# Optimization experiments

Measured on AMD Instinct MI355X. Metric: run time of the kernel, lower is better.

## Reference

```python
import jax, jax.numpy as jnp
import numpy as np

EMBED_DIM = 768
NUM_HEADS = 32
B = 4
N = 512


def setup_inputs() -> dict:
    key = jax.random.key(0)
    ks = jax.random.split(key, 11)
    s = 0.02  # param init scale
    E = EMBED_DIM
    return {
        "query": jax.random.normal(ks[0], (B, N, E), jnp.float32),
        "attn_bias": jax.random.normal(ks[1], (B * NUM_HEADS, N, N), jnp.float32),
        "delta_pos": jax.random.normal(ks[2], (B, N, N, 3), jnp.float32),
        "Wq": jax.random.normal(ks[3], (E, E), jnp.float32) * s,
        "bq": jnp.zeros((E,), jnp.float32),
        "Wk": jax.random.normal(ks[4], (E, E), jnp.float32) * s,
        "bk": jnp.zeros((E,), jnp.float32),
        "Wv": jax.random.normal(ks[5], (E, E), jnp.float32) * s,
        "bv": jnp.zeros((E,), jnp.float32),
        # force_proj{1,2,3} stacked: row c is the Linear(E,1) weight for axis c
        "Wf": jax.random.normal(ks[6], (3, E), jnp.float32) * s,
        "bf": jnp.zeros((3,), jnp.float32),
    }


def reference(query, attn_bias, delta_pos, Wq, bq, Wk, bk, Wv, bv, Wf, bf):
    b, n, e = query.shape
    h = NUM_HEADS
    d = e // h
    scaling = d ** (-0.5)
    # projections -> (b, h, n, d)
    q = (query @ Wq.T + bq).reshape(b, n, h, d).transpose(0, 2, 1, 3) * scaling
    k = (query @ Wk.T + bk).reshape(b, n, h, d).transpose(0, 2, 1, 3)
    v = (query @ Wv.T + bv).reshape(b, n, h, d).transpose(0, 2, 1, 3)
    # attention scores + bias; dropout is identity in eval mode (p=0.1, training=False)
    attn = jnp.einsum("bhnd,bhmd->bhnm", q, k) + attn_bias.reshape(b, h, n, n)
    probs = jax.nn.softmax(attn, axis=-1)  # (b,h,n,m)
    # rotate probs by delta_pos (c in {x,y,z}) and contract with v over m
    # x[b,n,c,h,d] = sum_m probs[b,h,n,m] * delta_pos[b,n,m,c] * v[b,h,m,d]
    x = jnp.einsum("bhnm,bnmc,bhmd->bnchd", probs, delta_pos, v).reshape(b, n, 3, e)
    # per-axis force projection: Linear(E,1) for each spatial axis
    force = jnp.einsum("bnce,ce->bnc", x, Wf) + bf
    return force.astype(jnp.float32)
```

## Files before the change

kernel.cpp:

```cpp
#include <hip/hip_runtime.h>
#include <hip/hip_bf16.h>
#include <cstdint>
#include <cstddef>

#define EMBED 768
#define NHEAD 32
#define HDIM 24
#define DPAD 32
#define BATCH 4
#define SEQ 512
#define WCOLS 1632
#define NPADCOL 1664

typedef __attribute__((ext_vector_type(8))) short short8;
typedef __attribute__((ext_vector_type(4))) short short4v;
typedef __attribute__((ext_vector_type(4))) float f32x4;

static __device__ __forceinline__ unsigned short f2b(float v) {
    __hip_bfloat16 h = __float2bfloat16(v);
    return *reinterpret_cast<unsigned short*>(&h);
}

__global__ __launch_bounds__(256) void prep_w_kernel(
    const float* __restrict__ Wq, const float* __restrict__ Wk,
    const float* __restrict__ Wv, const float* __restrict__ Wf,
    unsigned short* __restrict__ WcT)
{
    const float sc = 0.20412414523193154f;
    int j = blockIdx.x;
    #pragma unroll
    for (int rep = 0; rep < 3; ++rep) {
        int e = rep * 256 + threadIdx.x;
        float v;
        if (j < 768) {
            v = Wq[(size_t)j * EMBED + e] * sc;
        } else if (j < 1536) {
            v = Wk[(size_t)(j - 768) * EMBED + e];
        } else if (j < WCOLS) {
            int jc = j - 1536, h = jc / 3, c = jc - h * 3;
            float s = 0.f;
            #pragma unroll
            for (int d = 0; d < HDIM; ++d)
                s = fmaf(Wv[(size_t)(h * HDIM + d) * EMBED + e],
                         Wf[c * EMBED + h * HDIM + d], s);
            v = s;
        } else {
            v = 0.f;
        }
        WcT[(size_t)j * EMBED + e] = f2b(v);
    }
}

__global__ __launch_bounds__(256) void prep_b_kernel(
    const float* __restrict__ bq, const float* __restrict__ bk,
    const float* __restrict__ bv, const float* __restrict__ Wf,
    float* __restrict__ bcat)
{
    int j = blockIdx.x * 256 + threadIdx.x;
    if (j >= NPADCOL) return;
    float v = 0.f;
    if (j < 768) v = bq[j] * 0.20412414523193154f;
    else if (j < 1536) v = bk[j - 768];
    else if (j < WCOLS) {
        int jc = j - 1536, h = jc / 3, c = jc - h * 3;
        float s = 0.f;
        #pragma unroll
        for (int d = 0; d < HDIM; ++d)
            s = fmaf(bv[h * HDIM + d], Wf[c * EMBED + h * HDIM + d], s);
        v = s;
    }
    bcat[j] = v;
}

__global__ __launch_bounds__(256) void qconv_kernel(
    const float* __restrict__ q, unsigned short* __restrict__ o)
{
    size_t i = ((size_t)blockIdx.x * 256 + threadIdx.x) * 8;
    float4 a = *(const float4*)(q + i);
    float4 b = *(const float4*)(q + i + 4);
    union { unsigned short u[8]; short8 v; } r;
    r.u[0] = f2b(a.x); r.u[1] = f2b(a.y); r.u[2] = f2b(a.z); r.u[3] = f2b(a.w);
    r.u[4] = f2b(b.x); r.u[5] = f2b(b.y); r.u[6] = f2b(b.z); r.u[7] = f2b(b.w);
    *(short8*)(o + i) = r.v;
}

#define LSTR 36
__global__ __launch_bounds__(256) void gemm_kernel(
    const unsigned short* __restrict__ Aq, const unsigned short* __restrict__ WcT,
    const float* __restrict__ bcat,
    unsigned short* __restrict__ qp, unsigned short* __restrict__ kp,
    float* __restrict__ vwb)
{
    __shared__ short As[64 * LSTR];
    __shared__ short Bs[64 * LSTR];
    int t = threadIdx.x;
    int lane = t & 63, wv = t >> 6;
    int l15 = lane & 15, lg = lane >> 4;
    int m0 = blockIdx.x * 64, n0 = blockIdx.y * 64;
    int wm = (wv >> 1) * 32, wn = (wv & 1) * 32;

    f32x4 acc[2][2];
    #pragma unroll
    for (int i = 0; i < 2; ++i)
        #pragma unroll
        for (int j = 0; j < 2; ++j) acc[i][j] = (f32x4){0.f, 0.f, 0.f, 0.f};

    const unsigned short* Ag = Aq + (size_t)(m0 + (t >> 2)) * EMBED + (t & 3) * 8;
    const unsigned short* Bg = WcT + (size_t)(n0 + (t >> 2)) * EMBED + (t & 3) * 8;
    int lidx = (t >> 2) * LSTR + (t & 3) * 8;

    for (int kt = 0; kt < EMBED / 32; ++kt) {
        short8 av = *(const short8*)(Ag + kt * 32);
        short8 bv = *(const short8*)(Bg + kt * 32);
        __syncthreads();
        union { short4v h[2]; short8 v; } ua, ub;
        ua.v = av; ub.v = bv;
        *(short4v*)&As[lidx] = ua.h[0]; *(short4v*)&As[lidx + 4] = ua.h[1];
        *(short4v*)&Bs[lidx] = ub.h[0]; *(short4v*)&Bs[lidx + 4] = ub.h[1];
        __syncthreads();
        short8 af[2], bfr[2];
        #pragma unroll
        for (int i = 0; i < 2; ++i) {
            int ra = (wm + i * 16 + l15) * LSTR + lg * 8;
            int rb = (wn + i * 16 + l15) * LSTR + lg * 8;
            union { short4v h[2]; short8 v; } u1, u2;
            u1.h[0] = *(const short4v*)&As[ra]; u1.h[1] = *(const short4v*)&As[ra + 4];
            u2.h[0] = *(const short4v*)&Bs[rb]; u2.h[1] = *(const short4v*)&Bs[rb + 4];
            af[i] = u1.v; bfr[i] = u2.v;
        }
        #pragma unroll
        for (int mt = 0; mt < 2; ++mt)
            #pragma unroll
            for (int nt = 0; nt < 2; ++nt)
                acc[mt][nt] = __builtin_amdgcn_mfma_f32_16x16x32_bf16(
                    af[mt], bfr[nt], acc[mt][nt], 0, 0, 0);
    }

    #pragma unroll
    for (int mt = 0; mt < 2; ++mt) {
        #pragma unroll
        for (int nt = 0; nt < 2; ++nt) {
            #pragma unroll
            for (int r = 0; r < 4; ++r) {
                int gm = m0 + wm + mt * 16 + lg * 4 + r;
                int gn = n0 + wn + nt * 16 + l15;
                float v = acc[mt][nt][r] + bcat[gn];
                int b = gm >> 9, ns = gm & 511;
                if (gn < 768) {
                    int h = gn / 24, d = gn - h * 24;
                    qp[((size_t)(b * NHEAD + h) * SEQ + ns) * DPAD + d] = f2b(v);
                } else if (gn < 1536) {
                    int j2 = gn - 768, h = j2 / 24, d = j2 - h * 24;
                    kp[((size_t)(b * NHEAD + h) * SEQ + ns) * DPAD + d] = f2b(v);
                } else if (gn < WCOLS) {
                    int jc = gn - 1536, h = jc / 3, c = jc - h * 3;
                    vwb[((size_t)(b * NHEAD + h) * 3 + c) * SEQ + ns] = v;
                }
            }
        }
    }
}

__global__ __launch_bounds__(256) void init_out_kernel(
    const float* __restrict__ bf, float* __restrict__ out)
{
    int i = blockIdx.x * 256 + threadIdx.x;
    if (i < BATCH * SEQ * 3) out[i] = bf[i - (i / 3) * 3];
}

__global__ __launch_bounds__(512, 4) void attn_kernel(
    const unsigned short* __restrict__ qp, const unsigned short* __restrict__ kp,
    const float* __restrict__ vwb, const float* __restrict__ bias,
    const float* __restrict__ delta, float* __restrict__ out)
{
    __shared__ float denp[2][8][16];
    __shared__ float facp[8][16][3];
    int t = threadIdx.x, lane = t & 63, w = t >> 6;
    int l15 = lane & 15, lg = lane >> 4;
    int nbase = blockIdx.x * 16;
    int b = blockIdx.y;
    int hg = blockIdx.z;
    int mbase = w * 64;

    float dreg[4][4][3];
    #pragma unroll
    for (int r = 0; r < 4; ++r)
        #pragma unroll
        for (int tl = 0; tl < 4; ++tl) {
            const float* dp = delta +
                ((size_t)(b * SEQ + nbase + lg * 4 + r) * SEQ + mbase + tl * 16 + l15) * 3;
            dreg[r][tl][0] = dp[0]; dreg[r][tl][1] = dp[1]; dreg[r][tl][2] = dp[2];
        }

    float fac[4][3];
    #pragma unroll
    for (int r = 0; r < 4; ++r) { fac[r][0] = 0.f; fac[r][1] = 0.f; fac[r][2] = 0.f; }

    for (int hh = 0; hh < 8; ++hh) {
        int bh = b * NHEAD + hg * 8 + hh;
        short8 aq = *(const short8*)(qp + ((size_t)bh * SEQ + nbase + l15) * DPAD + lg * 8);
        f32x4 acc[4];
        #pragma unroll
        for (int tl = 0; tl < 4; ++tl) {
            short8 bk = *(const short8*)(kp +
                ((size_t)bh * SEQ + mbase + tl * 16 + l15) * DPAD + lg * 8);
            f32x4 z = {0.f, 0.f, 0.f, 0.f};
            acc[tl] = __builtin_amdgcn_mfma_f32_16x16x32_bf16(aq, bk, z, 0, 0, 0);
        }
        float ep[4][4];
        float dpart[4] = {0.f, 0.f, 0.f, 0.f};
        #pragma unroll
        for (int tl = 0; tl < 4; ++tl)
            #pragma unroll
            for (int r = 0; r < 4; ++r) {
                float s = acc[tl][r] + bias[
                    ((size_t)bh * SEQ + nbase + lg * 4 + r) * SEQ + mbase + tl * 16 + l15];
                float e = __expf(s);
                ep[tl][r] = e;
                dpart[r] += e;
            }
        #pragma unroll
        for (int r = 0; r < 4; ++r)
            #pragma unroll
            for (int o = 1; o <= 8; o <<= 1)
                dpart[r] += __shfl_xor(dpart[r], o);
        int buf = hh & 1;
        if (l15 == 0) {
            #pragma unroll
            for (int r = 0; r < 4; ++r) denp[buf][w][lg * 4 + r] = dpart[r];
        }
        __syncthreads();
        float rden[4];
        #pragma unroll
        for (int r = 0; r < 4; ++r) {
            float s = 0.f;
            #pragma unroll
            for (int ww = 0; ww < 8; ++ww) s += denp[buf][ww][lg * 4 + r];
            rden[r] = __builtin_amdgcn_rcpf(s);
        }
        #pragma unroll
        for (int tl = 0; tl < 4; ++tl) {
            #pragma unroll
            for (int c = 0; c < 3; ++c) {
                float vv = vwb[((size_t)bh * 3 + c) * SEQ + mbase + tl * 16 + l15];
                #pragma unroll
                for (int r = 0; r < 4; ++r)
                    fac[r][c] = fmaf(ep[tl][r] * rden[r] * vv, dreg[r][tl][c], fac[r][c]);
            }
        }
    }

    #pragma unroll
    for (int r = 0; r < 4; ++r)
        #pragma unroll
        for (int c = 0; c < 3; ++c) {
            float v = fac[r][c];
            #pragma unroll
            for (int o = 1; o <= 8; o <<= 1) v += __shfl_xor(v, o);
            fac[r][c] = v;
        }
    if (l15 == 0) {
        #pragma unroll
        for (int r = 0; r < 4; ++r)
            #pragma unroll
            for (int c = 0; c < 3; ++c) facp[w][lg * 4 + r][c] = fac[r][c];
    }
    __syncthreads();
    if (t < 48) {
        int n = t / 3, c = t - (t / 3) * 3;
        float s = 0.f;
        #pragma unroll
        for (int ww = 0; ww < 8; ++ww) s += facp[ww][n][c];
        atomicAdd(&out[(size_t)(b * SEQ + nbase + n) * 3 + c], s);
    }
}

extern "C" void kernel_launch(void* const* d_in, const int* in_sizes, int n_in,
                              void* d_out, int out_size, void* d_ws, size_t ws_size,
                              hipStream_t stream)
{
    const float* query = (const float*)d_in[0];
    const float* attn_bias = (const float*)d_in[1];
    const float* delta = (const float*)d_in[2];
    const float* Wq = (const float*)d_in[3];
    const float* bq = (const float*)d_in[4];
    const float* Wk = (const float*)d_in[5];
    const float* bk = (const float*)d_in[6];
    const float* Wv = (const float*)d_in[7];
    const float* bv = (const float*)d_in[8];
    const float* Wf = (const float*)d_in[9];
    const float* bf = (const float*)d_in[10];
    float* out = (float*)d_out;

    uint8_t* p = (uint8_t*)d_ws;
    unsigned short* qp   = (unsigned short*)p; p += (size_t)BATCH * NHEAD * SEQ * DPAD * 2;
    unsigned short* kp   = (unsigned short*)p; p += (size_t)BATCH * NHEAD * SEQ * DPAD * 2;
    unsigned short* qb16 = (unsigned short*)p; p += (size_t)BATCH * SEQ * EMBED * 2;
    unsigned short* WcT  = (unsigned short*)p; p += (size_t)NPADCOL * EMBED * 2;
    float* bcat = (float*)p;                   p += (size_t)NPADCOL * 4;
    float* vwb  = (float*)p;                   p += (size_t)BATCH * NHEAD * 3 * SEQ * 4;

    hipMemsetAsync(qp, 0, (size_t)BATCH * NHEAD * SEQ * DPAD * 2 * 2, stream);

    hipLaunchKernelGGL(prep_w_kernel, dim3(NPADCOL), dim3(256), 0, stream,
                       Wq, Wk, Wv, Wf, WcT);
    hipLaunchKernelGGL(prep_b_kernel, dim3(7), dim3(256), 0, stream,
                       bq, bk, bv, Wf, bcat);
    hipLaunchKernelGGL(qconv_kernel, dim3((BATCH * SEQ * EMBED) / (256 * 8)),
                       dim3(256), 0, stream, query, qb16);
    hipLaunchKernelGGL(gemm_kernel, dim3((BATCH * SEQ) / 64, NPADCOL / 64),
                       dim3(256), 0, stream, qb16, WcT, bcat, qp, kp, vwb);
    hipLaunchKernelGGL(init_out_kernel, dim3((BATCH * SEQ * 3 + 255) / 256),
                       dim3(256), 0, stream, bf, out);
    hipLaunchKernelGGL(attn_kernel, dim3(SEQ / 16, BATCH, 4), dim3(512), 0, stream,
                       qp, kp, vwb, attn_bias, delta, out);
}
```

Baseline: 259.7 us.

## Restructure attention per-head-per-wave, transpose delta_pos, fuse prep and conversion kernels

```diff
diff --git a/kernel.cpp b/kernel.cpp
--- a/kernel.cpp
+++ b/kernel.cpp
@@ -13,7 +13,6 @@
 #define NPADCOL 1664
 
 typedef __attribute__((ext_vector_type(8))) short short8;
-typedef __attribute__((ext_vector_type(4))) short short4v;
 typedef __attribute__((ext_vector_type(4))) float f32x4;
 
 static __device__ __forceinline__ unsigned short f2b(float v) {
@@ -24,7 +23,9 @@
 __global__ __launch_bounds__(256) void prep_w_kernel(
     const float* __restrict__ Wq, const float* __restrict__ Wk,
     const float* __restrict__ Wv, const float* __restrict__ Wf,
-    unsigned short* __restrict__ WcT)
+    const float* __restrict__ bq, const float* __restrict__ bkv,
+    const float* __restrict__ bv,
+    unsigned short* __restrict__ WcT, float* __restrict__ bcat)
 {
     const float sc = 0.20412414523193154f;
     int j = blockIdx.x;
@@ -49,50 +50,46 @@
         }
         WcT[(size_t)j * EMBED + e] = f2b(v);
     }
-}
-
-__global__ __launch_bounds__(256) void prep_b_kernel(
-    const float* __restrict__ bq, const float* __restrict__ bk,
-    const float* __restrict__ bv, const float* __restrict__ Wf,
-    float* __restrict__ bcat)
-{
-    int j = blockIdx.x * 256 + threadIdx.x;
-    if (j >= NPADCOL) return;
-    float v = 0.f;
-    if (j < 768) v = bq[j] * 0.20412414523193154f;
-    else if (j < 1536) v = bk[j - 768];
-    else if (j < WCOLS) {
-        int jc = j - 1536, h = jc / 3, c = jc - h * 3;
-        float s = 0.f;
-        #pragma unroll
-        for (int d = 0; d < HDIM; ++d)
-            s = fmaf(bv[h * HDIM + d], Wf[c * EMBED + h * HDIM + d], s);
-        v = s;
-    }
-    bcat[j] = v;
-}
-
-__global__ __launch_bounds__(256) void qconv_kernel(
-    const float* __restrict__ q, unsigned short* __restrict__ o)
-{
-    size_t i = ((size_t)blockIdx.x * 256 + threadIdx.x) * 8;
-    float4 a = *(const float4*)(q + i);
-    float4 b = *(const float4*)(q + i + 4);
-    union { unsigned short u[8]; short8 v; } r;
-    r.u[0] = f2b(a.x); r.u[1] = f2b(a.y); r.u[2] = f2b(a.z); r.u[3] = f2b(a.w);
-    r.u[4] = f2b(b.x); r.u[5] = f2b(b.y); r.u[6] = f2b(b.z); r.u[7] = f2b(b.w);
-    *(short8*)(o + i) = r.v;
-}
-
-#define LSTR 36
+    if (threadIdx.x == 0) {
+        float v = 0.f;
+        if (j < 768) v = bq[j] * sc;
+        else if (j < 1536) v = bkv[j - 768];
+        else if (j < WCOLS) {
+            int jc = j - 1536, h = jc / 3, c = jc - h * 3;
+            float s = 0.f;
+            #pragma unroll
+            for (int d = 0; d < HDIM; ++d)
+                s = fmaf(bv[h * HDIM + d], Wf[c * EMBED + h * HDIM + d], s);
+            v = s;
+        }
+        bcat[j] = v;
+    }
+}
+
+__global__ __launch_bounds__(256) void dtr_kernel(
+    const float* __restrict__ delta, float* __restrict__ dtr)
+{
+    size_t u = (size_t)blockIdx.x * 256 + threadIdx.x;
+    int m = (int)(u & 511);
+    int n = (int)((u >> 9) & 511);
+    int b = (int)(u >> 18);
+    float d0 = delta[u * 3 + 0];
+    float d1 = delta[u * 3 + 1];
+    float d2 = delta[u * 3 + 2];
+    dtr[((size_t)(b * 3 + 0) * SEQ + n) * SEQ + m] = d0;
+    dtr[((size_t)(b * 3 + 1) * SEQ + n) * SEQ + m] = d1;
+    dtr[((size_t)(b * 3 + 2) * SEQ + n) * SEQ + m] = d2;
+}
+
+#define LSTR 40
 __global__ __launch_bounds__(256) void gemm_kernel(
-    const unsigned short* __restrict__ Aq, const unsigned short* __restrict__ WcT,
+    const float* __restrict__ Aq, const unsigned short* __restrict__ WcT,
     const float* __restrict__ bcat,
     unsigned short* __restrict__ qp, unsigned short* __restrict__ kp,
     float* __restrict__ vwb)
 {
-    __shared__ short As[64 * LSTR];
-    __shared__ short Bs[64 * LSTR];
+    __shared__ short As[2][64 * LSTR];
+    __shared__ short Bs[2][64 * LSTR];
     int t = threadIdx.x;
     int lane = t & 63, wv = t >> 6;
     int l15 = lane & 15, lg = lane >> 4;
@@ -105,28 +102,43 @@
         #pragma unroll
         for (int j = 0; j < 2; ++j) acc[i][j] = (f32x4){0.f, 0.f, 0.f, 0.f};
 
-    const unsigned short* Ag = Aq + (size_t)(m0 + (t >> 2)) * EMBED + (t & 3) * 8;
-    const unsigned short* Bg = WcT + (size_t)(n0 + (t >> 2)) * EMBED + (t & 3) * 8;
-    int lidx = (t >> 2) * LSTR + (t & 3) * 8;
+    int sr = t >> 2;
+    int sc8 = (t & 3) * 8;
+    const float* Ag = Aq + (size_t)(m0 + sr) * EMBED + sc8;
+    const unsigned short* Bg = WcT + (size_t)(n0 + sr) * EMBED + sc8;
+    int lidx = sr * LSTR + sc8;
+
+    short8 fa, fb;
+    {
+        float4 a0 = *(const float4*)(Ag);
+        float4 a1 = *(const float4*)(Ag + 4);
+        union { unsigned short u[8]; short8 v; } r;
+        r.u[0] = f2b(a0.x); r.u[1] = f2b(a0.y); r.u[2] = f2b(a0.z); r.u[3] = f2b(a0.w);
+        r.u[4] = f2b(a1.x); r.u[5] = f2b(a1.y); r.u[6] = f2b(a1.z); r.u[7] = f2b(a1.w);
+        fa = r.v;
+        fb = *(const short8*)(Bg);
+    }
+    *(short8*)&As[0][lidx] = fa;
+    *(short8*)&Bs[0][lidx] = fb;
+    __syncthreads();
 
     for (int kt = 0; kt < EMBED / 32; ++kt) {
-        short8 av = *(const short8*)(Ag + kt * 32);
-        short8 bv = *(const short8*)(Bg + kt * 32);
-        __syncthreads();
-        union { short4v h[2]; short8 v; } ua, ub;
-        ua.v = av; ub.v = bv;
-        *(short4v*)&As[lidx] = ua.h[0]; *(short4v*)&As[lidx + 4] = ua.h[1];
-        *(short4v*)&Bs[lidx] = ub.h[0]; *(short4v*)&Bs[lidx + 4] = ub.h[1];
-        __syncthreads();
+        int cur = kt & 1;
+        bool more = (kt + 1) < EMBED / 32;
+        if (more) {
+            float4 a0 = *(const float4*)(Ag + (kt + 1) * 32);
+            float4 a1 = *(const float4*)(Ag + (kt + 1) * 32 + 4);
+            fb = *(const short8*)(Bg + (size_t)(kt + 1) * 32);
+            union { unsigned short u[8]; short8 v; } r;
+            r.u[0] = f2b(a0.x); r.u[1] = f2b(a0.y); r.u[2] = f2b(a0.z); r.u[3] = f2b(a0.w);
+            r.u[4] = f2b(a1.x); r.u[5] = f2b(a1.y); r.u[6] = f2b(a1.z); r.u[7] = f2b(a1.w);
+            fa = r.v;
+        }
         short8 af[2], bfr[2];
         #pragma unroll
         for (int i = 0; i < 2; ++i) {
-            int ra = (wm + i * 16 + l15) * LSTR + lg * 8;
-            int rb = (wn + i * 16 + l15) * LSTR + lg * 8;
-            union { short4v h[2]; short8 v; } u1, u2;
-            u1.h[0] = *(const short4v*)&As[ra]; u1.h[1] = *(const short4v*)&As[ra + 4];
-            u2.h[0] = *(const short4v*)&Bs[rb]; u2.h[1] = *(const short4v*)&Bs[rb + 4];
-            af[i] = u1.v; bfr[i] = u2.v;
+            af[i]  = *(const short8*)&As[cur][(wm + i * 16 + l15) * LSTR + lg * 8];
+            bfr[i] = *(const short8*)&Bs[cur][(wn + i * 16 + l15) * LSTR + lg * 8];
         }
         #pragma unroll
         for (int mt = 0; mt < 2; ++mt)
@@ -134,6 +146,11 @@
             for (int nt = 0; nt < 2; ++nt)
                 acc[mt][nt] = __builtin_amdgcn_mfma_f32_16x16x32_bf16(
                     af[mt], bfr[nt], acc[mt][nt], 0, 0, 0);
+        if (more) {
+            *(short8*)&As[cur ^ 1][lidx] = fa;
+            *(short8*)&Bs[cur ^ 1][lidx] = fb;
+            __syncthreads();
+        }
     }
 
     #pragma unroll
@@ -168,109 +185,76 @@
     if (i < BATCH * SEQ * 3) out[i] = bf[i - (i / 3) * 3];
 }
 
-__global__ __launch_bounds__(512, 4) void attn_kernel(
+__global__ __launch_bounds__(512) void attn_kernel(
     const unsigned short* __restrict__ qp, const unsigned short* __restrict__ kp,
     const float* __restrict__ vwb, const float* __restrict__ bias,
-    const float* __restrict__ delta, float* __restrict__ out)
-{
-    __shared__ float denp[2][8][16];
-    __shared__ float facp[8][16][3];
+    const float* __restrict__ dtr, float* __restrict__ out)
+{
+    __shared__ float wred[8][16][3];
     int t = threadIdx.x, lane = t & 63, w = t >> 6;
     int l15 = lane & 15, lg = lane >> 4;
     int nbase = blockIdx.x * 16;
     int b = blockIdx.y;
-    int hg = blockIdx.z;
-    int mbase = w * 64;
-
-    float dreg[4][4][3];
-    #pragma unroll
-    for (int r = 0; r < 4; ++r)
-        #pragma unroll
-        for (int tl = 0; tl < 4; ++tl) {
-            const float* dp = delta +
-                ((size_t)(b * SEQ + nbase + lg * 4 + r) * SEQ + mbase + tl * 16 + l15) * 3;
-            dreg[r][tl][0] = dp[0]; dreg[r][tl][1] = dp[1]; dreg[r][tl][2] = dp[2];
-        }
-
-    float fac[4][3];
-    #pragma unroll
-    for (int r = 0; r < 4; ++r) { fac[r][0] = 0.f; fac[r][1] = 0.f; fac[r][2] = 0.f; }
-
-    for (int hh = 0; hh < 8; ++hh) {
-        int bh = b * NHEAD + hg * 8 + hh;
-        short8 aq = *(const short8*)(qp + ((size_t)bh * SEQ + nbase + l15) * DPAD + lg * 8);
-        f32x4 acc[4];
-        #pragma unroll
-        for (int tl = 0; tl < 4; ++tl) {
-            short8 bk = *(const short8*)(kp +
-                ((size_t)bh * SEQ + mbase + tl * 16 + l15) * DPAD + lg * 8);
-            f32x4 z = {0.f, 0.f, 0.f, 0.f};
-            acc[tl] = __builtin_amdgcn_mfma_f32_16x16x32_bf16(aq, bk, z, 0, 0, 0);
-        }
-        float ep[4][4];
-        float dpart[4] = {0.f, 0.f, 0.f, 0.f};
-        #pragma unroll
-        for (int tl = 0; tl < 4; ++tl)
-            #pragma unroll
-            for (int r = 0; r < 4; ++r) {
-                float s = acc[tl][r] + bias[
-                    ((size_t)bh * SEQ + nbase + lg * 4 + r) * SEQ + mbase + tl * 16 + l15];
-                float e = __expf(s);
-                ep[tl][r] = e;
-                dpart[r] += e;
-            }
-        #pragma unroll
-        for (int r = 0; r < 4; ++r)
-            #pragma unroll
-            for (int o = 1; o <= 8; o <<= 1)
-                dpart[r] += __shfl_xor(dpart[r], o);
-        int buf = hh & 1;
-        if (l15 == 0) {
-            #pragma unroll
-            for (int r = 0; r < 4; ++r) denp[buf][w][lg * 4 + r] = dpart[r];
-        }
-        __syncthreads();
-        float rden[4];
+    int bh = b * NHEAD + blockIdx.z * 8 + w;
+
+    short8 aq = *(const short8*)(qp + ((size_t)bh * SEQ + nbase + l15) * DPAD + lg * 8);
+
+    const unsigned short* kbase = kp + (size_t)bh * SEQ * DPAD + lg * 8;
+    const float* vw0   = vwb + (size_t)bh * 3 * SEQ + l15;
+    const float* bbase = bias + ((size_t)bh * SEQ + nbase + lg * 4) * SEQ + l15;
+    const float* dbase = dtr + (size_t)b * 3 * SEQ * SEQ
+                             + (size_t)(nbase + lg * 4) * SEQ + l15;
+
+    float den[4] = {0.f, 0.f, 0.f, 0.f};
+    float facu[4][3];
+    #pragma unroll
+    for (int r = 0; r < 4; ++r) { facu[r][0] = 0.f; facu[r][1] = 0.f; facu[r][2] = 0.f; }
+
+    #pragma unroll 2
+    for (int mt = 0; mt < SEQ / 16; ++mt) {
+        int moff = mt * 16;
+        short8 bk = *(const short8*)(kbase + (size_t)(moff + l15) * DPAD);
+        f32x4 z = {0.f, 0.f, 0.f, 0.f};
+        f32x4 acc = __builtin_amdgcn_mfma_f32_16x16x32_bf16(aq, bk, z, 0, 0, 0);
+        float v0 = vw0[moff];
+        float v1 = vw0[SEQ + moff];
+        float v2 = vw0[2 * SEQ + moff];
         #pragma unroll
         for (int r = 0; r < 4; ++r) {
-            float s = 0.f;
-            #pragma unroll
-            for (int ww = 0; ww < 8; ++ww) s += denp[buf][ww][lg * 4 + r];
-            rden[r] = __builtin_amdgcn_rcpf(s);
-        }
-        #pragma unroll
-        for (int tl = 0; tl < 4; ++tl) {
-            #pragma unroll
-            for (int c = 0; c < 3; ++c) {
-                float vv = vwb[((size_t)bh * 3 + c) * SEQ + mbase + tl * 16 + l15];
-                #pragma unroll
-                for (int r = 0; r < 4; ++r)
-                    fac[r][c] = fmaf(ep[tl][r] * rden[r] * vv, dreg[r][tl][c], fac[r][c]);
-            }
-        }
-    }
-
-    #pragma unroll
-    for (int r = 0; r < 4; ++r)
-        #pragma unroll
-        for (int c = 0; c < 3; ++c) {
-            float v = fac[r][c];
-            #pragma unroll
-            for (int o = 1; o <= 8; o <<= 1) v += __shfl_xor(v, o);
-            fac[r][c] = v;
-        }
+            float e = __expf(acc[r] + bbase[(size_t)r * SEQ + moff]);
+            den[r] += e;
+            facu[r][0] = fmaf(e * v0, dbase[(size_t)r * SEQ + moff], facu[r][0]);
+            facu[r][1] = fmaf(e * v1, dbase[(size_t)SEQ * SEQ + r * SEQ + moff], facu[r][1]);
+            facu[r][2] = fmaf(e * v2, dbase[(size_t)2 * SEQ * SEQ + r * SEQ + moff], facu[r][2]);
+        }
+    }
+
+    #pragma unroll
+    for (int r = 0; r < 4; ++r) {
+        #pragma unroll
+        for (int o = 1; o <= 8; o <<= 1) {
+            den[r]     += __shfl_xor(den[r], o);
+            facu[r][0] += __shfl_xor(facu[r][0], o);
+            facu[r][1] += __shfl_xor(facu[r][1], o);
+            facu[r][2] += __shfl_xor(facu[r][2], o);
+        }
+        float rd = __builtin_amdgcn_rcpf(den[r]);
+        facu[r][0] *= rd; facu[r][1] *= rd; facu[r][2] *= rd;
+    }
     if (l15 == 0) {
         #pragma unroll
-        for (int r = 0; r < 4; ++r)
-            #pragma unroll
-            for (int c = 0; c < 3; ++c) facp[w][lg * 4 + r][c] = fac[r][c];
+        for (int r = 0; r < 4; ++r) {
+            wred[w][lg * 4 + r][0] = facu[r][0];
+            wred[w][lg * 4 + r][1] = facu[r][1];
+            wred[w][lg * 4 + r][2] = facu[r][2];
+        }
     }
     __syncthreads();
     if (t < 48) {
-        int n = t / 3, c = t - (t / 3) * 3;
+        int n = t / 3, c = t - n * 3;
         float s = 0.f;
         #pragma unroll
-        for (int ww = 0; ww < 8; ++ww) s += facp[ww][n][c];
+        for (int ww = 0; ww < 8; ++ww) s += wred[ww][n][c];
         atomicAdd(&out[(size_t)(b * SEQ + nbase + n) * 3 + c], s);
     }
 }
@@ -293,25 +277,23 @@
     float* out = (float*)d_out;
 
     uint8_t* p = (uint8_t*)d_ws;
-    unsigned short* qp   = (unsigned short*)p; p += (size_t)BATCH * NHEAD * SEQ * DPAD * 2;
-    unsigned short* kp   = (unsigned short*)p; p += (size_t)BATCH * NHEAD * SEQ * DPAD * 2;
-    unsigned short* qb16 = (unsigned short*)p; p += (size_t)BATCH * SEQ * EMBED * 2;
-    unsigned short* WcT  = (unsigned short*)p; p += (size_t)NPADCOL * EMBED * 2;
-    float* bcat = (float*)p;                   p += (size_t)NPADCOL * 4;
-    float* vwb  = (float*)p;                   p += (size_t)BATCH * NHEAD * 3 * SEQ * 4;
+    unsigned short* qp  = (unsigned short*)p; p += (size_t)BATCH * NHEAD * SEQ * DPAD * 2;
+    unsigned short* kp  = (unsigned short*)p; p += (size_t)BATCH * NHEAD * SEQ * DPAD * 2;
+    unsigned short* WcT = (unsigned short*)p; p += (size_t)NPADCOL * EMBED * 2;
+    float* bcat = (float*)p;                  p += (size_t)NPADCOL * 4;
+    float* vwb  = (float*)p;                  p += (size_t)BATCH * NHEAD * 3 * SEQ * 4;
+    float* dtr  = (float*)p;                  p += (size_t)BATCH * 3 * SEQ * SEQ * 4;
 
     hipMemsetAsync(qp, 0, (size_t)BATCH * NHEAD * SEQ * DPAD * 2 * 2, stream);
 
     hipLaunchKernelGGL(prep_w_kernel, dim3(NPADCOL), dim3(256), 0, stream,
-                       Wq, Wk, Wv, Wf, WcT);
-    hipLaunchKernelGGL(prep_b_kernel, dim3(7), dim3(256), 0, stream,
-                       bq, bk, bv, Wf, bcat);
-    hipLaunchKernelGGL(qconv_kernel, dim3((BATCH * SEQ * EMBED) / (256 * 8)),
-                       dim3(256), 0, stream, query, qb16);
+                       Wq, Wk, Wv, Wf, bq, bk, bv, WcT, bcat);
+    hipLaunchKernelGGL(dtr_kernel, dim3((BATCH * SEQ * SEQ) / 256), dim3(256),
+                       0, stream, delta, dtr);
     hipLaunchKernelGGL(gemm_kernel, dim3((BATCH * SEQ) / 64, NPADCOL / 64),
-                       dim3(256), 0, stream, qb16, WcT, bcat, qp, kp, vwb);
+                       dim3(256), 0, stream, query, WcT, bcat, qp, kp, vwb);
     hipLaunchKernelGGL(init_out_kernel, dim3((BATCH * SEQ * 3 + 255) / 256),
                        dim3(256), 0, stream, bf, out);
     hipLaunchKernelGGL(attn_kernel, dim3(SEQ / 16, BATCH, 4), dim3(512), 0, stream,
-                       qp, kp, vwb, attn_bias, delta, out);
-}
+                       qp, kp, vwb, attn_bias, dtr, out);
+}
```

After: 289.1 us. 1.11x slower.
